# Kernel tuning notes

Hardware: AMD Instinct MI355X
Metric: run time of the kernel (lower is better)

Reference implementation:

```python
import jax, jax.numpy as jnp
import numpy as np

B, S, D, H = 2, 2048, 1024, 16
HD = D // H  # 64

def setup_inputs() -> dict:
    key = jax.random.key(0)
    k1, k2, k3, k4, k5 = jax.random.split(key, 5)
    scale = 0.02
    return {
        "hidden_states": jax.random.normal(k1, (B, S, D), dtype=jnp.float32),
        "w_attn": jax.random.normal(k2, (D, 3 * D), dtype=jnp.float32) * scale,
        "b_attn": jax.random.normal(k3, (3 * D,), dtype=jnp.float32) * scale,
        "w_proj": jax.random.normal(k4, (D, D), dtype=jnp.float32) * scale,
        "b_proj": jax.random.normal(k5, (D,), dtype=jnp.float32) * scale,
    }

def reference(hidden_states, w_attn, b_attn, w_proj, b_proj):
    # qkv projection: [B,S,3D] -> split
    qkv = hidden_states @ w_attn + b_attn
    q, k, v = jnp.split(qkv, 3, axis=-1)
    # split heads -> [B,H,S,HD]
    def split_heads(t):
        return t.reshape(B, S, H, HD).transpose(0, 2, 1, 3)
    q, k, v = split_heads(q), split_heads(k), split_heads(v)
    # eager attention: full [B,H,S,S] scores, causal mask, softmax, AV
    scores = jnp.einsum('bhqd,bhkd->bhqk', q, k) / jnp.sqrt(jnp.float32(HD))
    causal = jnp.tril(jnp.ones((S, S), dtype=bool))  # [S,S]
    mask_value = jnp.finfo(scores.dtype).min
    scores = jnp.where(causal[None, None], scores, mask_value)
    attn = jax.nn.softmax(scores, axis=-1)
    out = jnp.einsum('bhqk,bhkd->bhqd', attn, v)
    # merge heads -> [B,S,D], output projection
    out = out.transpose(0, 2, 1, 3).reshape(B, S, D)
    out = out @ w_proj + b_proj
    return out
```

## Files before the change

### kernel.cpp

```cpp
#include <hip/hip_runtime.h>
#include <hip/hip_bf16.h>
#include <math.h>
#include <stdint.h>

typedef unsigned short u16;
typedef __attribute__((ext_vector_type(8))) short bf16x8;
typedef __attribute__((ext_vector_type(4))) float f32x4;

#define MFMA16(A,B,C) __builtin_amdgcn_mfma_f32_16x16x32_bf16(A,B,C,0,0,0)
#define EXP2F(x) __builtin_amdgcn_exp2f(x)

#define BB 2
#define SS 2048
#define NT (BB*SS)

__device__ __forceinline__ u16 f2bf(float f) {
    union { float f; unsigned u; } c; c.f = f;
    unsigned r = c.u + 0x7FFF + ((c.u >> 16) & 1);
    return (u16)(r >> 16);
}
__device__ __forceinline__ float bf2f(u16 v) {
    union { unsigned u; float f; } c; c.u = ((unsigned)v) << 16;
    return c.f;
}

__device__ __forceinline__ void gl_lds16(const u16* g, u16* l) {
    __builtin_amdgcn_global_load_lds(
        (const __attribute__((address_space(1))) void*)(uintptr_t)g,
        (__attribute__((address_space(3))) void*)(uintptr_t)l, 16, 0, 0);
}

__global__ __launch_bounds__(256) void cast_bf16(const float* __restrict__ in,
                                                 u16* __restrict__ out, int n) {
    int i = (blockIdx.x * 256 + threadIdx.x) * 4;
    if (i < n) {
        float4 v = *(const float4*)&in[i];
        ushort4 o;
        o.x = f2bf(v.x); o.y = f2bf(v.y); o.z = f2bf(v.z); o.w = f2bf(v.w);
        *(ushort4*)&out[i] = o;
    }
}

__global__ __launch_bounds__(256) void transpose_cast(const float* __restrict__ in,
                                                      u16* __restrict__ out, int M) {
    __shared__ float tile[64][65];
    const int k0 = blockIdx.x * 64, m0 = blockIdx.y * 64;
    const int t = threadIdx.x;
    #pragma unroll
    for (int rep = 0; rep < 16; ++rep) {
        int idx = rep * 256 + t;
        int kk = idx >> 6, mm = idx & 63;
        tile[kk][mm] = in[(size_t)(k0 + kk) * M + m0 + mm];
    }
    __syncthreads();
    #pragma unroll
    for (int rep = 0; rep < 16; ++rep) {
        int idx = rep * 256 + t;
        int mm = idx >> 6, kk = idx & 63;
        out[(size_t)(m0 + mm) * 1024 + k0 + kk] = f2bf(tile[kk][mm]);
    }
}

__global__ __launch_bounds__(256) void transpose_v(const u16* __restrict__ qkvb,
                                                   u16* __restrict__ vtg) {
    __shared__ u16 tile[64][72];
    const int bh = blockIdx.x, kt = blockIdx.y;
    const int b = bh >> 4, h = bh & 15;
    const int t = threadIdx.x;
    const int tt = t >> 2;
    #pragma unroll
    for (int r = 0; r < 2; ++r) {
        int c = (t & 3) + r * 4;
        *(bf16x8*)&tile[tt][c * 8] =
            *(const bf16x8*)&qkvb[(size_t)(b * SS + kt * 64 + tt) * 3072 + 2048 + h * 64 + c * 8];
    }
    __syncthreads();
    u16* dst0 = vtg + ((size_t)bh * 32 + kt) * 4096;
    #pragma unroll
    for (int rep = 0; rep < 2; ++rep) {
        int flat = rep * 256 + t;
        int g = flat >> 6, d = flat & 63;
        int tok0 = (g >> 2) * 32 + (g & 3) * 4;
        ushort4 a, bb;
        a.x  = tile[tok0 + 0][d];  a.y  = tile[tok0 + 1][d];
        a.z  = tile[tok0 + 2][d];  a.w  = tile[tok0 + 3][d];
        bb.x = tile[tok0 + 16][d]; bb.y = tile[tok0 + 17][d];
        bb.z = tile[tok0 + 18][d]; bb.w = tile[tok0 + 19][d];
        u16* dst = dst0 + (size_t)flat * 8;
        *(ushort4*)dst = a;
        *(ushort4*)(dst + 4) = bb;
    }
}

template<int MD, typename OutT>
__global__ __launch_bounds__(256) void gemm_bt(const u16* __restrict__ A,
                                               const u16* __restrict__ BT,
                                               const float* __restrict__ bias,
                                               OutT* __restrict__ C) {
    __shared__ u16 As[128 * 32];
    __shared__ u16 Bs[128 * 32];
    const int t = threadIdx.x;
    const int lane = t & 63;
    const int w = t >> 6;
    const int wr = (w >> 1) * 64, wc = (w & 1) * 64;
    const int ln = lane & 15, hi = lane >> 4;
    const int n0 = blockIdx.x * 128;
    const int m0 = blockIdx.y * 128;

    f32x4 acc[4][4];
    const f32x4 fz = {0.f, 0.f, 0.f, 0.f};
    #pragma unroll
    for (int i = 0; i < 4; ++i)
        #pragma unroll
        for (int j = 0; j < 4; ++j) acc[i][j] = fz;

    const int srow_in = lane >> 2;
    const int schunk  = lane & 3;

    for (int k0 = 0; k0 < 1024; k0 += 32) {
        __syncthreads();
        #pragma unroll
        for (int p = 0; p < 2; ++p) {
            int q   = w * 2 + p;
            int row = q * 16 + srow_in;
            int cg  = schunk ^ (row & 3);
            gl_lds16(&A [(size_t)(n0 + row) * 1024 + k0 + cg * 8], &As[q * 512]);
            gl_lds16(&BT[(size_t)(m0 + row) * 1024 + k0 + cg * 8], &Bs[q * 512]);
        }
        __syncthreads();
        bf16x8 af[4], bf[4];
        #pragma unroll
        for (int mi = 0; mi < 4; ++mi) {
            int r = wr + mi * 16 + ln;
            af[mi] = *(const bf16x8*)&As[r * 32 + ((hi ^ (r & 3)) << 3)];
        }
        #pragma unroll
        for (int ni = 0; ni < 4; ++ni) {
            int r = wc + ni * 16 + ln;
            bf[ni] = *(const bf16x8*)&Bs[r * 32 + ((hi ^ (r & 3)) << 3)];
        }
        #pragma unroll
        for (int mi = 0; mi < 4; ++mi)
            #pragma unroll
            for (int ni = 0; ni < 4; ++ni)
                acc[mi][ni] = MFMA16(af[mi], bf[ni], acc[mi][ni]);
    }

    #pragma unroll
    for (int mi = 0; mi < 4; ++mi) {
        #pragma unroll
        for (int ni = 0; ni < 4; ++ni) {
            int col = m0 + wc + ni * 16 + ln;
            float bv = bias[col];
            #pragma unroll
            for (int r = 0; r < 4; ++r) {
                int row = n0 + wr + mi * 16 + hi * 4 + r;
                float v = acc[mi][ni][r] + bv;
                if constexpr (sizeof(OutT) == 4) C[(size_t)row * MD + col] = v;
                else                             C[(size_t)row * MD + col] = (OutT)f2bf(v);
            }
        }
    }
}

__global__ __launch_bounds__(256) void attn_mfma(const u16* __restrict__ qkv,
                                                 const u16* __restrict__ vtg,
                                                 u16* __restrict__ ctx) {
    __shared__ u16 Ks[2][64 * 64];
    __shared__ u16 Vs[2][64 * 64];
    const int bh = blockIdx.x;
    const int qt = 31 - blockIdx.y;
    const int b = bh >> 4, h = bh & 15;
    const int t = threadIdx.x, w = t >> 6, lane = t & 63;
    const int ln = lane & 15, hi = lane >> 4;
    const int qrow = qt * 64 + w * 16 + ln;
    const size_t tok = (size_t)b * SS;

    bf16x8 qb[2];
    #pragma unroll
    for (int t2 = 0; t2 < 2; ++t2) {
        bf16x8 v = *(const bf16x8*)&qkv[(tok + qrow) * 3072 + h * 64 + t2 * 32 + hi * 8];
        #pragma unroll
        for (int i = 0; i < 8; ++i)
            v[i] = (short)f2bf(bf2f((u16)v[i]) * 0.180336881f);
        qb[t2] = v;
    }

    float m_run = -1e30f, l_run = 0.f;
    f32x4 o[4];
    const f32x4 fz = {0.f, 0.f, 0.f, 0.f};
    #pragma unroll
    for (int i = 0; i < 4; ++i) o[i] = fz;

    const int kkey_l = w * 8 + (lane >> 3);
    const int ksch   = lane & 7;
    const u16* vsrc  = vtg + ((size_t)bh * 32) * 4096;

    {
        const size_t kvb = tok * 3072 + h * 64;
        #pragma unroll
        for (int p = 0; p < 2; ++p) {
            int kk = p * 32 + kkey_l;
            gl_lds16(&qkv[kvb + (size_t)kk * 3072 + 1024 + ((ksch ^ (kk & 7)) << 3)],
                     &Ks[0][(p * 32 + w * 8) * 64]);
            gl_lds16(&vsrc[(size_t)((w * 2 + p) * 64 + lane) * 8],
                     &Vs[0][(w * 2 + p) * 512]);
        }
    }

    for (int kt = 0; kt <= qt; ++kt) {
        const int cur = kt & 1;
        __syncthreads();

        if (kt < qt) {
            const int nxt = cur ^ 1;
            const size_t kvb = (tok + (kt + 1) * 64) * 3072 + h * 64;
            const u16* vs2 = vsrc + (size_t)(kt + 1) * 4096;
            #pragma unroll
            for (int p = 0; p < 2; ++p) {
                int kk = p * 32 + kkey_l;
                gl_lds16(&qkv[kvb + (size_t)kk * 3072 + 1024 + ((ksch ^ (kk & 7)) << 3)],
                         &Ks[nxt][(p * 32 + w * 8) * 64]);
                gl_lds16(&vs2[(size_t)((w * 2 + p) * 64 + lane) * 8],
                         &Vs[nxt][(w * 2 + p) * 512]);
            }
        }

        f32x4 sacc[4];
        __builtin_amdgcn_s_setprio(1);
        #pragma unroll
        for (int s = 0; s < 4; ++s) {
            int key = s * 16 + ln;
            f32x4 a = fz;
            #pragma unroll
            for (int t2 = 0; t2 < 2; ++t2) {
                bf16x8 kf = *(const bf16x8*)&Ks[cur][key * 64 + (((t2 * 4 + hi) ^ (key & 7)) << 3)];
                a = MFMA16(kf, qb[t2], a);
            }
            sacc[s] = a;
        }
        __builtin_amdgcn_s_setprio(0);

        float p_[16];
        float mloc = -1e30f;
        if (kt == qt) {
            #pragma unroll
            for (int s = 0; s < 4; ++s)
                #pragma unroll
                for (int r = 0; r < 4; ++r) {
                    int keyg = kt * 64 + s * 16 + hi * 4 + r;
                    float v = (keyg <= qrow) ? sacc[s][r] : -1e30f;
                    p_[s * 4 + r] = v;
                    mloc = fmaxf(mloc, v);
                }
        } else {
            #pragma unroll
            for (int s = 0; s < 4; ++s)
                #pragma unroll
                for (int r = 0; r < 4; ++r) {
                    float v = sacc[s][r];
                    p_[s * 4 + r] = v;
                    mloc = fmaxf(mloc, v);
                }
        }
        mloc = fmaxf(mloc, __shfl_xor(mloc, 16));
        mloc = fmaxf(mloc, __shfl_xor(mloc, 32));
        if (!__all(mloc - m_run <= 8.f)) {
            float m_new = fmaxf(m_run, mloc);
            float alpha = EXP2F(m_run - m_new);
            l_run *= alpha;
            #pragma unroll
            for (int dt = 0; dt < 4; ++dt) o[dt] *= alpha;
            m_run = m_new;
        }
        float lsum = 0.f;
        #pragma unroll
        for (int i = 0; i < 16; ++i) {
            float e = EXP2F(p_[i] - m_run);
            p_[i] = e;
            lsum += e;
        }
        lsum += __shfl_xor(lsum, 16);
        lsum += __shfl_xor(lsum, 32);
        l_run += lsum;

        bf16x8 pa[2];
        #pragma unroll
        for (int k2 = 0; k2 < 2; ++k2) {
            union { unsigned wd[4]; bf16x8 v; } pu;
            #pragma unroll
            for (int qi = 0; qi < 4; ++qi)
                asm("v_cvt_pk_bf16_f32 %0, %1, %2"
                    : "=v"(pu.wd[qi])
                    : "v"(p_[k2 * 8 + 2 * qi]), "v"(p_[k2 * 8 + 2 * qi + 1]));
            pa[k2] = pu.v;
        }

        __builtin_amdgcn_s_setprio(1);
        #pragma unroll
        for (int dt = 0; dt < 4; ++dt)
            #pragma unroll
            for (int k2 = 0; k2 < 2; ++k2) {
                bf16x8 va = *(const bf16x8*)&Vs[cur][(size_t)((k2 * 4 + hi) * 64 + dt * 16 + ln) * 8];
                o[dt] = MFMA16(va, pa[k2], o[dt]);
            }
        __builtin_amdgcn_s_setprio(0);
    }

    float inv = 1.f / l_run;
    #pragma unroll
    for (int dt = 0; dt < 4; ++dt) {
        ushort4 ov;
        ov.x = f2bf(o[dt][0] * inv);
        ov.y = f2bf(o[dt][1] * inv);
        ov.z = f2bf(o[dt][2] * inv);
        ov.w = f2bf(o[dt][3] * inv);
        *(ushort4*)&ctx[(tok + qrow) * 1024 + h * 64 + dt * 16 + hi * 4] = ov;
    }
}

extern "C" void kernel_launch(void* const* d_in, const int* in_sizes, int n_in,
                              void* d_out, int out_size, void* d_ws, size_t ws_size,
                              hipStream_t stream) {
    const float* hs     = (const float*)d_in[0];
    const float* w_attn = (const float*)d_in[1];
    const float* b_attn = (const float*)d_in[2];
    const float* w_proj = (const float*)d_in[3];
    const float* b_proj = (const float*)d_in[4];
    float* out = (float*)d_out;

    char* ws = (char*)d_ws;
    u16* hsb  = (u16*)ws;
    u16* waT  = (u16*)(ws + ((size_t)8  << 20));
    u16* wpT  = (u16*)(ws + ((size_t)14 << 20));
    u16* qkvb = (u16*)(ws + ((size_t)16 << 20));
    u16* ctxb = (u16*)(ws + ((size_t)40 << 20));
    u16* vtg  = (u16*)(ws + ((size_t)48 << 20));

    cast_bf16<<<4096, 256, 0, stream>>>(hs, hsb, NT * 1024);
    transpose_cast<<<dim3(16, 48), 256, 0, stream>>>(w_attn, waT, 3072);
    transpose_cast<<<dim3(16, 16), 256, 0, stream>>>(w_proj, wpT, 1024);

    gemm_bt<3072, u16><<<dim3(NT / 128, 3072 / 128), 256, 0, stream>>>(hsb, waT, b_attn, qkvb);
    transpose_v<<<dim3(BB * 16, SS / 64), 256, 0, stream>>>(qkvb, vtg);
    attn_mfma<<<dim3(BB * 16, SS / 64), 256, 0, stream>>>(qkvb, vtg, ctxb);
    gemm_bt<1024, float><<<dim3(NT / 128, 1024 / 128), 256, 0, stream>>>(ctxb, wpT, b_proj, out);
}
```

Baseline: 111.3 us.

## Fuse V transpose into QKV GEMM epilogue, widen attention to 128-row blocks

The QKV GEMM epilogue now writes V directly in the transposed tile layout that attention expects, which removes the separate transpose_v kernel. The two weight transpose launches are merged into one. Attention blocks now use 512 threads covering 128 query rows and share each K/V tile load across 8 waves, with per-wave causal skipping and a reordered block schedule. Fewer launches and less K/V reload traffic are traded for larger blocks and more divergence in the causal tail.

```diff
diff --git a/kernel.cpp b/kernel.cpp
--- a/kernel.cpp
+++ b/kernel.cpp
@@ -41,10 +41,17 @@
     }
 }
 
-__global__ __launch_bounds__(256) void transpose_cast(const float* __restrict__ in,
-                                                      u16* __restrict__ out, int M) {
+__global__ __launch_bounds__(256) void transpose_weights(const float* __restrict__ wa,
+                                                         const float* __restrict__ wp,
+                                                         u16* __restrict__ waT,
+                                                         u16* __restrict__ wpT) {
     __shared__ float tile[64][65];
-    const int k0 = blockIdx.x * 64, m0 = blockIdx.y * 64;
+    const int k0 = blockIdx.x * 64;
+    const bool isA = blockIdx.y < 48;
+    const int m0 = (isA ? blockIdx.y : blockIdx.y - 48) * 64;
+    const int M = isA ? 3072 : 1024;
+    const float* in = isA ? wa : wp;
+    u16* out = isA ? waT : wpT;
     const int t = threadIdx.x;
     #pragma unroll
     for (int rep = 0; rep < 16; ++rep) {
@@ -61,42 +68,12 @@
     }
 }
 
-__global__ __launch_bounds__(256) void transpose_v(const u16* __restrict__ qkvb,
-                                                   u16* __restrict__ vtg) {
-    __shared__ u16 tile[64][72];
-    const int bh = blockIdx.x, kt = blockIdx.y;
-    const int b = bh >> 4, h = bh & 15;
-    const int t = threadIdx.x;
-    const int tt = t >> 2;
-    #pragma unroll
-    for (int r = 0; r < 2; ++r) {
-        int c = (t & 3) + r * 4;
-        *(bf16x8*)&tile[tt][c * 8] =
-            *(const bf16x8*)&qkvb[(size_t)(b * SS + kt * 64 + tt) * 3072 + 2048 + h * 64 + c * 8];
-    }
-    __syncthreads();
-    u16* dst0 = vtg + ((size_t)bh * 32 + kt) * 4096;
-    #pragma unroll
-    for (int rep = 0; rep < 2; ++rep) {
-        int flat = rep * 256 + t;
-        int g = flat >> 6, d = flat & 63;
-        int tok0 = (g >> 2) * 32 + (g & 3) * 4;
-        ushort4 a, bb;
-        a.x  = tile[tok0 + 0][d];  a.y  = tile[tok0 + 1][d];
-        a.z  = tile[tok0 + 2][d];  a.w  = tile[tok0 + 3][d];
-        bb.x = tile[tok0 + 16][d]; bb.y = tile[tok0 + 17][d];
-        bb.z = tile[tok0 + 18][d]; bb.w = tile[tok0 + 19][d];
-        u16* dst = dst0 + (size_t)flat * 8;
-        *(ushort4*)dst = a;
-        *(ushort4*)(dst + 4) = bb;
-    }
-}
-
-template<int MD, typename OutT>
+template<int MD, typename OutT, bool FUSE_V>
 __global__ __launch_bounds__(256) void gemm_bt(const u16* __restrict__ A,
                                                const u16* __restrict__ BT,
                                                const float* __restrict__ bias,
-                                               OutT* __restrict__ C) {
+                                               OutT* __restrict__ C,
+                                               u16* __restrict__ vtg) {
     __shared__ u16 As[128 * 32];
     __shared__ u16 Bs[128 * 32];
     const int t = threadIdx.x;
@@ -152,28 +129,46 @@
         for (int ni = 0; ni < 4; ++ni) {
             int col = m0 + wc + ni * 16 + ln;
             float bv = bias[col];
-            #pragma unroll
-            for (int r = 0; r < 4; ++r) {
-                int row = n0 + wr + mi * 16 + hi * 4 + r;
-                float v = acc[mi][ni][r] + bv;
-                if constexpr (sizeof(OutT) == 4) C[(size_t)row * MD + col] = v;
-                else                             C[(size_t)row * MD + col] = (OutT)f2bf(v);
+            int row0 = n0 + wr + mi * 16 + hi * 4;
+            if (FUSE_V && col >= 2048) {
+                int b  = row0 >> 11;
+                int s  = row0 & 2047;
+                int kt = s >> 6, kl = s & 63;
+                int h  = (col - 2048) >> 6, d = (col - 2048) & 63;
+                int g    = (kl >> 5) * 4 + ((kl >> 2) & 3);
+                int half = (kl >> 4) & 1;
+                ushort4 ov;
+                ov.x = f2bf(acc[mi][ni][0] + bv);
+                ov.y = f2bf(acc[mi][ni][1] + bv);
+                ov.z = f2bf(acc[mi][ni][2] + bv);
+                ov.w = f2bf(acc[mi][ni][3] + bv);
+                *(ushort4*)&vtg[(size_t)((b * 16 + h) * 32 + kt) * 4096 +
+                                (size_t)(g * 64 + d) * 8 + half * 4] = ov;
+            } else {
+                #pragma unroll
+                for (int r = 0; r < 4; ++r) {
+                    float v = acc[mi][ni][r] + bv;
+                    if constexpr (sizeof(OutT) == 4) C[(size_t)(row0 + r) * MD + col] = v;
+                    else                             C[(size_t)(row0 + r) * MD + col] = (OutT)f2bf(v);
+                }
             }
         }
     }
 }
 
-__global__ __launch_bounds__(256) void attn_mfma(const u16* __restrict__ qkv,
+__global__ __launch_bounds__(512) void attn_mfma(const u16* __restrict__ qkv,
                                                  const u16* __restrict__ vtg,
                                                  u16* __restrict__ ctx) {
     __shared__ u16 Ks[2][64 * 64];
     __shared__ u16 Vs[2][64 * 64];
     const int bh = blockIdx.x;
-    const int qt = 31 - blockIdx.y;
+    const int y  = blockIdx.y;
+    const int qt = (y < 8) ? (15 - y) : (y - 8);
     const int b = bh >> 4, h = bh & 15;
     const int t = threadIdx.x, w = t >> 6, lane = t & 63;
     const int ln = lane & 15, hi = lane >> 4;
-    const int qrow = qt * 64 + w * 16 + ln;
+    const int qrow = qt * 128 + w * 16 + ln;
+    const int wrow0 = qt * 128 + w * 16;
     const size_t tok = (size_t)b * SS;
 
     bf16x8 qb[2];
@@ -192,39 +187,33 @@
     #pragma unroll
     for (int i = 0; i < 4; ++i) o[i] = fz;
 
-    const int kkey_l = w * 8 + (lane >> 3);
-    const int ksch   = lane & 7;
-    const u16* vsrc  = vtg + ((size_t)bh * 32) * 4096;
+    const int kkey = w * 8 + (lane >> 3);
+    const int ksch = lane & 7;
+    const u16* vsrc = vtg + ((size_t)bh * 32) * 4096;
+    const int ktmax = 2 * qt + 1;
 
     {
         const size_t kvb = tok * 3072 + h * 64;
-        #pragma unroll
-        for (int p = 0; p < 2; ++p) {
-            int kk = p * 32 + kkey_l;
-            gl_lds16(&qkv[kvb + (size_t)kk * 3072 + 1024 + ((ksch ^ (kk & 7)) << 3)],
-                     &Ks[0][(p * 32 + w * 8) * 64]);
-            gl_lds16(&vsrc[(size_t)((w * 2 + p) * 64 + lane) * 8],
-                     &Vs[0][(w * 2 + p) * 512]);
-        }
-    }
-
-    for (int kt = 0; kt <= qt; ++kt) {
+        gl_lds16(&qkv[kvb + (size_t)kkey * 3072 + 1024 + ((ksch ^ (kkey & 7)) << 3)],
+                 &Ks[0][w * 512]);
+        gl_lds16(&vsrc[(size_t)(w * 64 + lane) * 8], &Vs[0][w * 512]);
+    }
+
+    for (int kt = 0; kt <= ktmax; ++kt) {
         const int cur = kt & 1;
         __syncthreads();
 
-        if (kt < qt) {
+        if (kt < ktmax) {
             const int nxt = cur ^ 1;
             const size_t kvb = (tok + (kt + 1) * 64) * 3072 + h * 64;
-            const u16* vs2 = vsrc + (size_t)(kt + 1) * 4096;
-            #pragma unroll
-            for (int p = 0; p < 2; ++p) {
-                int kk = p * 32 + kkey_l;
-                gl_lds16(&qkv[kvb + (size_t)kk * 3072 + 1024 + ((ksch ^ (kk & 7)) << 3)],
-                         &Ks[nxt][(p * 32 + w * 8) * 64]);
-                gl_lds16(&vs2[(size_t)((w * 2 + p) * 64 + lane) * 8],
-                         &Vs[nxt][(w * 2 + p) * 512]);
-            }
-        }
+            gl_lds16(&qkv[kvb + (size_t)kkey * 3072 + 1024 + ((ksch ^ (kkey & 7)) << 3)],
+                     &Ks[nxt][w * 512]);
+            gl_lds16(&vsrc[(size_t)(kt + 1) * 4096 + (size_t)(w * 64 + lane) * 8],
+                     &Vs[nxt][w * 512]);
+        }
+
+        if (kt * 64 > wrow0 + 15) continue;
+        const bool needMask = (kt * 64 + 63 > wrow0);
 
         f32x4 sacc[4];
         __builtin_amdgcn_s_setprio(1);
@@ -243,7 +232,7 @@
 
         float p_[16];
         float mloc = -1e30f;
-        if (kt == qt) {
+        if (needMask) {
             #pragma unroll
             for (int s = 0; s < 4; ++s)
                 #pragma unroll
@@ -338,11 +327,9 @@
     u16* vtg  = (u16*)(ws + ((size_t)48 << 20));
 
     cast_bf16<<<4096, 256, 0, stream>>>(hs, hsb, NT * 1024);
-    transpose_cast<<<dim3(16, 48), 256, 0, stream>>>(w_attn, waT, 3072);
-    transpose_cast<<<dim3(16, 16), 256, 0, stream>>>(w_proj, wpT, 1024);
-
-    gemm_bt<3072, u16><<<dim3(NT / 128, 3072 / 128), 256, 0, stream>>>(hsb, waT, b_attn, qkvb);
-    transpose_v<<<dim3(BB * 16, SS / 64), 256, 0, stream>>>(qkvb, vtg);
-    attn_mfma<<<dim3(BB * 16, SS / 64), 256, 0, stream>>>(qkvb, vtg, ctxb);
-    gemm_bt<1024, float><<<dim3(NT / 128, 1024 / 128), 256, 0, stream>>>(ctxb, wpT, b_proj, out);
-}
+    transpose_weights<<<dim3(16, 64), 256, 0, stream>>>(w_attn, w_proj, waT, wpT);
+
+    gemm_bt<3072, u16, true><<<dim3(NT / 128, 3072 / 128), 256, 0, stream>>>(hsb, waT, b_attn, qkvb, vtg);
+    attn_mfma<<<dim3(BB * 16, 16), 512, 0, stream>>>(qkvb, vtg, ctxb);
+    gemm_bt<1024, float, false><<<dim3(NT / 128, 1024 / 128), 256, 0, stream>>>(ctxb, wpT, b_proj, out, nullptr);
+}
```

After: 122.4 us. +10.0%, slower.
